# Optimization experiments

Measured on AMD Instinct MI355X. Metric: run time of the kernel, lower is better.

Reference implementation:

```python
import jax, jax.numpy as jnp
import numpy as np

NUM_EXPERTS = 8
CAPACITY_FACTOR = 1.25


def setup_inputs() -> dict:
    key = jax.random.key(0)
    kx, kw = jax.random.split(key)
    x = jax.random.normal(kx, (8, 4096, 1024), dtype=jnp.float32)
    W = jax.random.normal(kw, (NUM_EXPERTS, 1024), dtype=jnp.float32) * (1.0 / np.sqrt(1024))
    return {"x": x, "W": W, "force_top_k": 2}


def reference(x, W, force_top_k):
    # Eval-mode router: no gate noise, no expert dropout (expert_dropout=0.0).
    B, S, D = x.shape
    num_tokens = B * S
    top_k = min(force_top_k, NUM_EXPERTS)

    x_flat = x.reshape(num_tokens, D)                       # [N, D]
    router_logits = x_flat @ W.T                            # [N, E]

    probs = jax.nn.softmax(router_logits, axis=-1)          # [N, E]
    dispatch_weights, expert_indices = jax.lax.top_k(probs, top_k)  # [N, k]

    total_capacity = int(num_tokens * top_k * CAPACITY_FACTOR)
    per_expert_capacity = max(1, total_capacity // NUM_EXPERTS)

    # one_hot(expert_indices).sum over k -> per-token expert mask [N, E]
    expert_mask = jax.nn.one_hot(expert_indices, NUM_EXPERTS, dtype=jnp.int32).sum(axis=1)
    tokens_per_expert = expert_mask.sum(axis=0).astype(jnp.float32)  # [E]
    capacity_mask = tokens_per_expert > per_expert_capacity
    num_dropped = capacity_mask.sum()

    avg_probs = probs.mean(axis=0)                          # [E]
    load_balance_loss = jnp.sum(
        tokens_per_expert / max(1, num_tokens) * avg_probs
    ) * NUM_EXPERTS

    log_probs = jax.nn.log_softmax(router_logits, axis=-1)
    entropy = -(probs * log_probs).sum(axis=-1).mean()
    target_entropy = jnp.log(jnp.float32(NUM_EXPERTS))
    router_entropy_loss = jnp.maximum(target_entropy - entropy, 0.0)

    expert_usage = tokens_per_expert / max(1, num_tokens)

    return (dispatch_weights, expert_indices, router_logits,
            load_balance_loss, router_entropy_loss, num_dropped, expert_usage)
```

## Files before the change

kernel.cpp:

```cpp
#include <hip/hip_runtime.h>

#define NTOK 32768
#define D 1024
#define NE 8

template<int CTRL>
__device__ __forceinline__ float dpp_row_add(float v) {
    int r = __builtin_amdgcn_update_dpp(0, __float_as_int(v), CTRL, 0xf, 0xf, true);
    return v + __int_as_float(r);
}

__device__ __forceinline__ float row_reduce_add(float v) {
    v = dpp_row_add<0x121>(v);
    v = dpp_row_add<0x122>(v);
    v = dpp_row_add<0x124>(v);
    v = dpp_row_add<0x128>(v);
    return v;
}

__device__ __forceinline__ float wave_reduce_add(float v) {
    v = row_reduce_add(v);
    v += __shfl_xor(v, 16, 64);
    v += __shfl_xor(v, 32, 64);
    return v;
}

__global__ __launch_bounds__(256, 2) void logits_kernel(
        const float* __restrict__ x, const float* __restrict__ W,
        float* __restrict__ logits) {
    const int lane = threadIdx.x & 63;
    const int wid  = (blockIdx.x * blockDim.x + threadIdx.x) >> 6;
    const int nw   = (gridDim.x * blockDim.x) >> 6;

    float4 w[NE][4];
#pragma unroll
    for (int e = 0; e < NE; ++e)
#pragma unroll
        for (int c = 0; c < 4; ++c)
            w[e][c] = *(const float4*)(W + e * D + c * 256 + lane * 4);

    int t = wid;
    float4 xq[4];
    if (t < NTOK) {
        const float* xr = x + (size_t)t * D + lane * 4;
#pragma unroll
        for (int c = 0; c < 4; ++c) xq[c] = *(const float4*)(xr + c * 256);
    }

    while (t < NTOK) {
        const int tn = t + nw;
        float4 xn[4];
        if (tn < NTOK) {
            const float* xr = x + (size_t)tn * D + lane * 4;
#pragma unroll
            for (int c = 0; c < 4; ++c) xn[c] = *(const float4*)(xr + c * 256);
        }

        float acc[NE];
#pragma unroll
        for (int e = 0; e < NE; ++e) {
            float s = 0.f;
#pragma unroll
            for (int c = 0; c < 4; ++c) {
                s = fmaf(xq[c].x, w[e][c].x, s);
                s = fmaf(xq[c].y, w[e][c].y, s);
                s = fmaf(xq[c].z, w[e][c].z, s);
                s = fmaf(xq[c].w, w[e][c].w, s);
            }
            acc[e] = row_reduce_add(s);
        }

        const int k = lane & 7;
        float b0 = (k & 1) ? acc[1] : acc[0];
        float b1 = (k & 1) ? acc[3] : acc[2];
        float b2 = (k & 1) ? acc[5] : acc[4];
        float b3 = (k & 1) ? acc[7] : acc[6];
        float c0 = (k & 2) ? b1 : b0;
        float c1 = (k & 2) ? b3 : b2;
        float v  = (k & 4) ? c1 : c0;
        v += __shfl_xor(v, 16, 64);
        v += __shfl_xor(v, 32, 64);

        if (lane < NE) logits[t * NE + lane] = v;

        t = tn;
#pragma unroll
        for (int c = 0; c < 4; ++c) xq[c] = xn[c];
    }
}

__global__ __launch_bounds__(256) void router_kernel(
        const float* __restrict__ logits, float* __restrict__ dw,
        float* __restrict__ eidx, float* __restrict__ ws) {
    __shared__ float s_acc[17];
    const int tid = threadIdx.x;
    if (tid < 17) s_acc[tid] = 0.f;
    __syncthreads();

    const int t = blockIdx.x * 256 + tid;
    float l[8];
    const float4 a = *(const float4*)(logits + t * 8);
    const float4 b = *(const float4*)(logits + t * 8 + 4);
    l[0] = a.x; l[1] = a.y; l[2] = a.z; l[3] = a.w;
    l[4] = b.x; l[5] = b.y; l[6] = b.z; l[7] = b.w;

    float m = l[0];
#pragma unroll
    for (int e = 1; e < 8; ++e) m = fmaxf(m, l[e]);
    float p[8], S = 0.f;
#pragma unroll
    for (int e = 0; e < 8; ++e) { p[e] = __expf(l[e] - m); S += p[e]; }
    const float inv = 1.0f / S;
#pragma unroll
    for (int e = 0; e < 8; ++e) p[e] *= inv;

    int e1 = 0; float p1 = p[0];
#pragma unroll
    for (int e = 1; e < 8; ++e) if (p[e] > p1) { p1 = p[e]; e1 = e; }
    int e2 = -1; float p2 = -1.f;
#pragma unroll
    for (int e = 0; e < 8; ++e) if (e != e1 && p[e] > p2) { p2 = p[e]; e2 = e; }

    dw[t * 2 + 0]   = p1;
    dw[t * 2 + 1]   = p2;
    eidx[t * 2 + 0] = (float)e1;
    eidx[t * 2 + 1] = (float)e2;

    const float logS = __logf(S);
    float ent = 0.f;
#pragma unroll
    for (int e = 0; e < 8; ++e) ent -= p[e] * (l[e] - m - logS);

    const bool lead = ((tid & 63) == 0);
#pragma unroll
    for (int e = 0; e < 8; ++e) {
        float r = wave_reduce_add(p[e]);
        if (lead) atomicAdd(&s_acc[e], r);
    }
#pragma unroll
    for (int e = 0; e < 8; ++e) {
        float r = wave_reduce_add((float)((e1 == e) + (e2 == e)));
        if (lead) atomicAdd(&s_acc[8 + e], r);
    }
    {
        float r = wave_reduce_add(ent);
        if (lead) atomicAdd(&s_acc[16], r);
    }
    __syncthreads();
    if (tid < 17) atomicAdd(&ws[tid], s_acc[tid]);
}

__global__ void finalize_kernel(const float* __restrict__ ws,
                                float* __restrict__ outs) {
    if (threadIdx.x == 0 && blockIdx.x == 0) {
        const float invN = 1.0f / 32768.0f;
        float lbl = 0.f, dropped = 0.f;
#pragma unroll
        for (int e = 0; e < 8; ++e) {
            const float cnt = ws[8 + e];
            const float avg = ws[e] * invN;
            lbl += (cnt * invN) * avg;
            if (cnt > 10240.0f) dropped += 1.f;
            outs[3 + e] = cnt * invN;
        }
        outs[0] = lbl * 8.0f;
        const float ent = ws[16] * invN;
        outs[1] = fmaxf(2.0794415416798357f - ent, 0.0f);
        outs[2] = dropped;
    }
}

extern "C" void kernel_launch(void* const* d_in, const int* in_sizes, int n_in,
                              void* d_out, int out_size, void* d_ws, size_t ws_size,
                              hipStream_t stream) {
    const float* x = (const float*)d_in[0];
    const float* W = (const float*)d_in[1];
    float* out     = (float*)d_out;

    float* dw      = out;
    float* eidx    = out + 65536;
    float* logits  = out + 131072;
    float* scalars = out + 393216;
    float* ws      = (float*)d_ws;

    hipMemsetAsync(d_ws, 0, 32 * sizeof(float), stream);
    logits_kernel<<<512, 256, 0, stream>>>(x, W, logits);
    router_kernel<<<128, 256, 0, stream>>>(logits, dw, eidx, ws);
    finalize_kernel<<<1, 64, 0, stream>>>(ws, scalars);
}
```

Measured before the change: 200.4 us.

## Fuse softmax/top-k router into logits kernel with per-wave partial sums

The softmax, top-2 selection, entropy and per-expert statistics now run inside the logits kernel, computed across each 8-lane group with DPP max/add and ballots. This removes the separate router kernel, its re-read of the logits, and the memset. Each wave writes 17 partial sums to the workspace and a single-block finalize kernel reduces them, replacing global atomics. The trade-off is extra ALU work and cross-lane ops in the bandwidth-bound loop, and ties now resolve to the lowest index through the ballot.

After: 199.3 us. About the same (-0.5%).

```diff
diff --git a/kernel.cpp b/kernel.cpp
--- a/kernel.cpp
+++ b/kernel.cpp
@@ -3,18 +3,19 @@
 #define NTOK 32768
 #define D 1024
 #define NE 8
+#define NWAVES 2048
 
 template<int CTRL>
-__device__ __forceinline__ float dpp_row_add(float v) {
-    int r = __builtin_amdgcn_update_dpp(0, __float_as_int(v), CTRL, 0xf, 0xf, true);
-    return v + __int_as_float(r);
+__device__ __forceinline__ float dpp_ror(float v) {
+    return __int_as_float(
+        __builtin_amdgcn_update_dpp(0, __float_as_int(v), CTRL, 0xf, 0xf, true));
 }
 
 __device__ __forceinline__ float row_reduce_add(float v) {
-    v = dpp_row_add<0x121>(v);
-    v = dpp_row_add<0x122>(v);
-    v = dpp_row_add<0x124>(v);
-    v = dpp_row_add<0x128>(v);
+    v += dpp_ror<0x121>(v);
+    v += dpp_ror<0x122>(v);
+    v += dpp_ror<0x124>(v);
+    v += dpp_ror<0x128>(v);
     return v;
 }
 
@@ -25,12 +26,33 @@
     return v;
 }
 
-__global__ __launch_bounds__(256, 2) void logits_kernel(
+__device__ __forceinline__ float grp8_add(float v) {
+    v += dpp_ror<0x121>(v);
+    v += dpp_ror<0x122>(v);
+    v += dpp_ror<0x124>(v);
+    return v;
+}
+__device__ __forceinline__ float grp8_max(float v) {
+    v = fmaxf(v, dpp_ror<0x121>(v));
+    v = fmaxf(v, dpp_ror<0x122>(v));
+    v = fmaxf(v, dpp_ror<0x124>(v));
+    return v;
+}
+__device__ __forceinline__ float red_per_expert(float v) {
+    v += dpp_ror<0x128>(v);
+    v += __shfl_xor(v, 16, 64);
+    v += __shfl_xor(v, 32, 64);
+    return v;
+}
+
+__global__ __launch_bounds__(256, 2) void fused_kernel(
         const float* __restrict__ x, const float* __restrict__ W,
-        float* __restrict__ logits) {
+        float* __restrict__ logits, float* __restrict__ dw,
+        float* __restrict__ eidx, float* __restrict__ ws) {
     const int lane = threadIdx.x & 63;
     const int wid  = (blockIdx.x * blockDim.x + threadIdx.x) >> 6;
     const int nw   = (gridDim.x * blockDim.x) >> 6;
+    const int k    = lane & 7;
 
     float4 w[NE][4];
 #pragma unroll
@@ -38,6 +60,8 @@
 #pragma unroll
         for (int c = 0; c < 4; ++c)
             w[e][c] = *(const float4*)(W + e * D + c * 256 + lane * 4);
+
+    float p_acc = 0.f, c_acc = 0.f, ent_acc = 0.f;
 
     int t = wid;
     float4 xq[4];
@@ -70,7 +94,6 @@
             acc[e] = row_reduce_add(s);
         }
 
-        const int k = lane & 7;
         float b0 = (k & 1) ? acc[1] : acc[0];
         float b1 = (k & 1) ? acc[3] : acc[2];
         float b2 = (k & 1) ? acc[5] : acc[4];
@@ -81,90 +104,74 @@
         v += __shfl_xor(v, 16, 64);
         v += __shfl_xor(v, 32, 64);
 
-        if (lane < NE) logits[t * NE + lane] = v;
+        const float m    = grp8_max(v);
+        const float pe   = __expf(v - m);
+        const float S    = grp8_add(pe);
+        const float p    = pe / S;
+        const float logS = __logf(S);
+
+        const float m1 = grp8_max(p);
+        const unsigned long long b1m = __ballot(p == m1);
+        const int e1 = __ffsll(b1m & 0xffull) - 1;
+        const float cand = (k == e1) ? -1.0f : p;
+        const float m2 = grp8_max(cand);
+        const unsigned long long b2m = __ballot(cand == m2);
+        const int e2 = __ffsll(b2m & 0xffull) - 1;
+
+        if (lane < 8)       logits[t * 8 + lane] = v;
+        if (lane == 0)      *(float2*)(dw   + t * 2) = make_float2(m1, m2);
+        else if (lane == 1) *(float2*)(eidx + t * 2) = make_float2((float)e1, (float)e2);
+
+        p_acc   += p;
+        c_acc   += (float)((k == e1) + (k == e2));
+        ent_acc += p * (v - m - logS);
 
         t = tn;
 #pragma unroll
         for (int c = 0; c < 4; ++c) xq[c] = xn[c];
     }
+
+    const float pr = red_per_expert(p_acc) * 0.125f;
+    const float cr = red_per_expert(c_acc) * 0.125f;
+    const float er = wave_reduce_add(ent_acc) * -0.125f;
+    const float outv = (lane < 8) ? pr : ((lane < 16) ? cr : er);
+    if (lane < 17) ws[wid * 17 + lane] = outv;
 }
 
-__global__ __launch_bounds__(256) void router_kernel(
-        const float* __restrict__ logits, float* __restrict__ dw,
-        float* __restrict__ eidx, float* __restrict__ ws) {
+__global__ __launch_bounds__(256) void finalize_kernel(
+        const float* __restrict__ ws, float* __restrict__ outs) {
     __shared__ float s_acc[17];
     const int tid = threadIdx.x;
     if (tid < 17) s_acc[tid] = 0.f;
     __syncthreads();
 
-    const int t = blockIdx.x * 256 + tid;
-    float l[8];
-    const float4 a = *(const float4*)(logits + t * 8);
-    const float4 b = *(const float4*)(logits + t * 8 + 4);
-    l[0] = a.x; l[1] = a.y; l[2] = a.z; l[3] = a.w;
-    l[4] = b.x; l[5] = b.y; l[6] = b.z; l[7] = b.w;
-
-    float m = l[0];
+    float loc[17];
 #pragma unroll
-    for (int e = 1; e < 8; ++e) m = fmaxf(m, l[e]);
-    float p[8], S = 0.f;
+    for (int i = 0; i < 17; ++i) loc[i] = 0.f;
+    for (int w = tid; w < NWAVES; w += 256) {
+        const float* p = ws + w * 17;
 #pragma unroll
-    for (int e = 0; e < 8; ++e) { p[e] = __expf(l[e] - m); S += p[e]; }
-    const float inv = 1.0f / S;
-#pragma unroll
-    for (int e = 0; e < 8; ++e) p[e] *= inv;
-
-    int e1 = 0; float p1 = p[0];
-#pragma unroll
-    for (int e = 1; e < 8; ++e) if (p[e] > p1) { p1 = p[e]; e1 = e; }
-    int e2 = -1; float p2 = -1.f;
-#pragma unroll
-    for (int e = 0; e < 8; ++e) if (e != e1 && p[e] > p2) { p2 = p[e]; e2 = e; }
-
-    dw[t * 2 + 0]   = p1;
-    dw[t * 2 + 1]   = p2;
-    eidx[t * 2 + 0] = (float)e1;
-    eidx[t * 2 + 1] = (float)e2;
-
-    const float logS = __logf(S);
-    float ent = 0.f;
-#pragma unroll
-    for (int e = 0; e < 8; ++e) ent -= p[e] * (l[e] - m - logS);
-
-    const bool lead = ((tid & 63) == 0);
-#pragma unroll
-    for (int e = 0; e < 8; ++e) {
-        float r = wave_reduce_add(p[e]);
-        if (lead) atomicAdd(&s_acc[e], r);
+        for (int i = 0; i < 17; ++i) loc[i] += p[i];
     }
 #pragma unroll
-    for (int e = 0; e < 8; ++e) {
-        float r = wave_reduce_add((float)((e1 == e) + (e2 == e)));
-        if (lead) atomicAdd(&s_acc[8 + e], r);
-    }
-    {
-        float r = wave_reduce_add(ent);
-        if (lead) atomicAdd(&s_acc[16], r);
+    for (int i = 0; i < 17; ++i) {
+        const float r = wave_reduce_add(loc[i]);
+        if ((tid & 63) == 0) atomicAdd(&s_acc[i], r);
     }
     __syncthreads();
-    if (tid < 17) atomicAdd(&ws[tid], s_acc[tid]);
-}
 
-__global__ void finalize_kernel(const float* __restrict__ ws,
-                                float* __restrict__ outs) {
-    if (threadIdx.x == 0 && blockIdx.x == 0) {
+    if (tid == 0) {
         const float invN = 1.0f / 32768.0f;
         float lbl = 0.f, dropped = 0.f;
 #pragma unroll
         for (int e = 0; e < 8; ++e) {
-            const float cnt = ws[8 + e];
-            const float avg = ws[e] * invN;
-            lbl += (cnt * invN) * avg;
+            const float cnt = s_acc[8 + e];
+            lbl += (cnt * invN) * (s_acc[e] * invN);
             if (cnt > 10240.0f) dropped += 1.f;
             outs[3 + e] = cnt * invN;
         }
         outs[0] = lbl * 8.0f;
-        const float ent = ws[16] * invN;
+        const float ent = s_acc[16] * invN;
         outs[1] = fmaxf(2.0794415416798357f - ent, 0.0f);
         outs[2] = dropped;
     }
@@ -183,8 +190,6 @@
     float* scalars = out + 393216;
     float* ws      = (float*)d_ws;
 
-    hipMemsetAsync(d_ws, 0, 32 * sizeof(float), stream);
-    logits_kernel<<<512, 256, 0, stream>>>(x, W, logits);
-    router_kernel<<<128, 256, 0, stream>>>(logits, dw, eidx, ws);
-    finalize_kernel<<<1, 64, 0, stream>>>(ws, scalars);
+    fused_kernel<<<512, 256, 0, stream>>>(x, W, logits, dw, eidx, ws);
+    finalize_kernel<<<1, 256, 0, stream>>>(ws, scalars);
 }
```
